# Performance work log

Measured on AMD Instinct MI355X. Metric: run time of the kernel, lower is better.

## Reference

```python
import jax, jax.numpy as jnp
import numpy as np

N = 50000      # nodes
E = 800000     # edges (avg degree 16)
NODE = 64      # node_attr_size
EDGE = 16      # edge_attr_size
H = 2          # gat_heads
C = 64         # hidden_size (per-head out channels)
F = H * C      # feature_size = 128
L = 2          # num_gat_layers
K = 10         # num_clusters
EPS = 1e-5
NEG_SLOPE = 0.2


def setup_inputs() -> dict:
    key = jax.random.key(0)
    ks = jax.random.split(key, 16)
    s = 0.05
    inp = {
        "x": jax.random.normal(ks[0], (N, NODE), jnp.float32),
        "edge_index": jax.random.randint(ks[1], (2, E), 0, N, jnp.int64 if jax.config.read('jax_enable_x64') else jnp.int32),
        "edge_attr": jax.random.normal(ks[2], (E, EDGE), jnp.float32),
        # node_feat_proj
        "Wp": jax.random.normal(ks[3], (NODE, F), jnp.float32) * s,
        "bp": jnp.zeros((F,), jnp.float32),
        # per-layer LayerNorm affine params, stacked over layers
        "ln_g": jnp.ones((L, F), jnp.float32),
        "ln_b": jnp.zeros((L, F), jnp.float32),
        # per-layer GATv2Conv params (PyG: lin_l, lin_r with bias, lin_edge no bias, att, out bias)
        "Wl": jax.random.normal(ks[4], (L, F, F), jnp.float32) * s,
        "bl": jnp.zeros((L, F), jnp.float32),
        "Wr": jax.random.normal(ks[5], (L, F, F), jnp.float32) * s,
        "br": jnp.zeros((L, F), jnp.float32),
        "We": jax.random.normal(ks[6], (L, EDGE, F), jnp.float32) * s,
        "att": jax.random.normal(ks[7], (L, H, C), jnp.float32) * s,
        "bout": jnp.zeros((L, F), jnp.float32),
        # classifier
        "Wc": jax.random.normal(ks[8], (F, K), jnp.float32) * s,
        "bc": jnp.zeros((K,), jnp.float32),
    }
    return inp


def _layer_norm(x, g, b):
    mu = jnp.mean(x, axis=-1, keepdims=True)
    var = jnp.var(x, axis=-1, keepdims=True)
    return (x - mu) * jax.lax.rsqrt(var + EPS) * g + b


def _gatv2_conv(x, src, dst, Wl, bl, Wr, br, We, att, bout):
    # x: [N, F] -> out: [N, H*C]
    xl = (x @ Wl + bl).reshape(N, H, C)          # source transform
    xr = (x @ Wr + br).reshape(N, H, C)          # target transform
    ee = (jnp.zeros(0),)  # placeholder, edge emb computed by caller closure
    return xl, xr


def reference(x, edge_index, edge_attr, Wp, bp, ln_g, ln_b, Wl, bl, Wr, br, We, att, bout, Wc, bc):
    src, dst = edge_index[0], edge_index[1]
    h = x @ Wp + bp                                   # [N, F]
    for i in range(L):
        identity = h
        hn = _layer_norm(h, ln_g[i], ln_b[i])
        xl = (hn @ Wl[i] + bl[i]).reshape(N, H, C)    # lin_l(x)  (source side)
        xr = (hn @ Wr[i] + br[i]).reshape(N, H, C)    # lin_r(x)  (target side)
        ee = (edge_attr @ We[i]).reshape(E, H, C)     # lin_edge(edge_attr)
        m = xl[src] + xr[dst] + ee                    # [E, H, C]
        m = jnp.where(m > 0, m, NEG_SLOPE * m)        # LeakyReLU(0.2)
        logits = jnp.einsum('ehc,hc->eh', m, att[i])  # [E, H]
        # segment softmax over incoming edges of each target node
        mx = jax.ops.segment_max(logits, dst, num_segments=N)
        ex = jnp.exp(logits - mx[dst])
        den = jax.ops.segment_sum(ex, dst, num_segments=N)
        alpha = ex / den[dst]                         # [E, H]
        msg = xl[src] * alpha[:, :, None]             # [E, H, C]
        agg = jax.ops.segment_sum(msg, dst, num_segments=N)  # [N, H, C]
        hg = agg.reshape(N, F) + bout[i]
        h = jax.nn.relu(hg) + identity                # relu -> dropout(eval no-op) -> residual add
    node_embeddings = h
    classification_output = h @ Wc + bc               # [N, K]
    return (classification_output, node_embeddings)
```

## Files before the change

### kernel.cpp

```cpp
#include <hip/hip_runtime.h>
#include <math.h>

#define N_NODES 50000
#define N_EDGES 800000
#define FDIM 128
#define KCLS 10

typedef float v2f __attribute__((ext_vector_type(2)));

__device__ __forceinline__ v2f pksplat(float a) { v2f r; r.x = a; r.y = a; return r; }
__device__ __forceinline__ v2f pkfma(v2f a, v2f b, v2f c) { return __builtin_elementwise_fma(a, b, c); }
__device__ __forceinline__ v2f pklrelu(v2f v) {
    v2f z = pksplat(0.f);
    v2f mx = __builtin_elementwise_max(v, z);
    v2f mn = __builtin_elementwise_min(v, z);
    return pkfma(pksplat(0.2f), mn, mx);
}
__device__ __forceinline__ int rfl(int v) { return __builtin_amdgcn_readfirstlane(v); }

__device__ __forceinline__ float half_sum32(float x) {
    int v;
    v = __builtin_amdgcn_update_dpp(0, __float_as_int(x), 0xB1, 0xF, 0xF, true);
    x += __int_as_float(v);
    v = __builtin_amdgcn_update_dpp(0, __float_as_int(x), 0x4E, 0xF, 0xF, true);
    x += __int_as_float(v);
    v = __builtin_amdgcn_update_dpp(0, __float_as_int(x), 0x124, 0xF, 0xF, true);
    x += __int_as_float(v);
    v = __builtin_amdgcn_update_dpp(0, __float_as_int(x), 0x128, 0xF, 0xF, true);
    x += __int_as_float(v);
    v = __builtin_amdgcn_ds_swizzle(__float_as_int(x), 0x401F);
    x += __int_as_float(v);
    return x;
}


__global__ void k_count(const int* __restrict__ dst, int* __restrict__ indeg, int e_total) {
    int e = blockIdx.x * 256 + threadIdx.x;
    if (e < e_total) atomicAdd(&indeg[dst[e]], 1);
}

__global__ __launch_bounds__(1024) void k_scan_block(const int* __restrict__ in, int* __restrict__ excl,
                                                     int* __restrict__ bsum, int n) {
    __shared__ int sh[1024];
    int t = threadIdx.x;
    int g = blockIdx.x * 1024 + t;
    int v = (g < n) ? in[g] : 0;
    sh[t] = v;
    __syncthreads();
    for (int d = 1; d < 1024; d <<= 1) {
        int x = (t >= d) ? sh[t - d] : 0;
        __syncthreads();
        sh[t] += x;
        __syncthreads();
    }
    if (g < n) excl[g] = sh[t] - v;
    if (t == 1023) bsum[blockIdx.x] = sh[t];
}

__global__ void k_scan_small(int* bsum, int nb) {
    if (threadIdx.x == 0 && blockIdx.x == 0) {
        int run = 0;
        for (int i = 0; i < nb; i++) { int v = bsum[i]; bsum[i] = run; run += v; }
    }
}

__global__ __launch_bounds__(1024) void k_scan_add(int* __restrict__ offs, const int* __restrict__ bsum,
                                                   int* __restrict__ cursor, int n, int e_total) {
    int g = blockIdx.x * 1024 + threadIdx.x;
    if (g < n) {
        int v = offs[g] + bsum[blockIdx.x];
        offs[g] = v;
        cursor[g] = v;
    }
    if (g == 0) offs[n] = e_total;
}

__global__ void k_scatter_fused(const int* __restrict__ src, const int* __restrict__ dst,
                                const float* __restrict__ edge_attr,
                                int* __restrict__ cursor, int* __restrict__ ssrc,
                                float* __restrict__ sea, int e_total) {
    int e = blockIdx.x * 256 + threadIdx.x;
    if (e < e_total) {
        int d = dst[e];
        int p = atomicAdd(&cursor[d], 1);
        ssrc[p] = src[e];
        const float4* ea = (const float4*)&edge_attr[(size_t)e * 16];
        float4* out = (float4*)&sea[(size_t)p * 16];
        float4 a = ea[0], b = ea[1], c = ea[2], q = ea[3];
        out[0] = a; out[1] = b; out[2] = c; out[3] = q;
    }
}

__global__ void k_scatter(const int* __restrict__ src, const int* __restrict__ dst,
                          int* __restrict__ cursor, int* __restrict__ seid, int* __restrict__ ssrc, int e_total) {
    int e = blockIdx.x * 256 + threadIdx.x;
    if (e < e_total) {
        int d = dst[e];
        int p = atomicAdd(&cursor[d], 1);
        seid[p] = e;
        ssrc[p] = src[e];
    }
}


__global__ __launch_bounds__(256) void k_ln_gemm_first(const float* __restrict__ x, const float* __restrict__ Wp,
                                                       const float* __restrict__ bp,
                                                       const float* __restrict__ lng, const float* __restrict__ lnb,
                                                       const float* __restrict__ Wl, const float* __restrict__ bl,
                                                       const float* __restrict__ Wr, const float* __restrict__ br,
                                                       float* __restrict__ h, float* __restrict__ xl,
                                                       float* __restrict__ xr, int n) {
    __shared__ float u[10240];
    __shared__ float shn[4096];
    __shared__ float smu[32], srs[32];
    int t = threadIdx.x;
    int row0 = blockIdx.x * 32;
    int nrows = min(32, n - row0);
    float* shx = u;
    float* shwp = u + 2048;

    for (int i = t; i < 2048; i += 256)
        ((float4*)shwp)[i] = ((const float4*)Wp)[i];
    for (int i = t; i < 512; i += 256) {
        int r = i >> 4;
        float4 v = make_float4(0.f, 0.f, 0.f, 0.f);
        if (r < nrows) v = ((const float4*)x)[row0 * 16 + i];
        ((float4*)shx)[i] = v;
    }
    __syncthreads();

    int tr = (t >> 5) * 4;
    int tc = (t & 31) * 4;
    {
        float acc[4][4];
        float4 b4 = *(const float4*)&bp[tc];
#pragma unroll
        for (int j = 0; j < 4; j++) { acc[j][0] = b4.x; acc[j][1] = b4.y; acc[j][2] = b4.z; acc[j][3] = b4.w; }
        for (int k = 0; k < 64; k++) {
            float4 w = *(float4*)&shwp[k * 128 + tc];
#pragma unroll
            for (int j = 0; j < 4; j++) {
                float a = shx[(tr + j) * 64 + k];
                acc[j][0] = fmaf(a, w.x, acc[j][0]);
                acc[j][1] = fmaf(a, w.y, acc[j][1]);
                acc[j][2] = fmaf(a, w.z, acc[j][2]);
                acc[j][3] = fmaf(a, w.w, acc[j][3]);
            }
        }
#pragma unroll
        for (int j = 0; j < 4; j++) {
            int r = row0 + tr + j;
            float4 o = make_float4(acc[j][0], acc[j][1], acc[j][2], acc[j][3]);
            *(float4*)&shn[(tr + j) * 128 + tc] = o;
            if (r < n) *(float4*)&h[r * 128 + tc] = o;
        }
    }
    __syncthreads();

    {
        int r = t >> 3, sl = t & 7;
        float s = 0.f, ss = 0.f;
        for (int c = sl; c < 128; c += 8) {
            float v = shn[r * 128 + c];
            s += v; ss += v * v;
        }
#pragma unroll
        for (int o = 1; o < 8; o <<= 1) { s += __shfl_xor(s, o, 64); ss += __shfl_xor(ss, o, 64); }
        if (sl == 0) {
            float mu = s * (1.f / 128.f);
            float var = ss * (1.f / 128.f) - mu * mu;
            smu[r] = mu;
            srs[r] = rsqrtf(var + 1e-5f);
        }
    }
    __syncthreads();
    for (int i = t; i < 4096; i += 256) {
        int r = i >> 7, c = i & 127;
        shn[i] = (shn[i] - smu[r]) * srs[r] * lng[c] + lnb[c];
    }

    float accl[4][4], accr[4][4];
    {
        float4 bl4 = *(const float4*)&bl[tc];
        float4 br4 = *(const float4*)&br[tc];
#pragma unroll
        for (int j = 0; j < 4; j++) {
            accl[j][0] = bl4.x; accl[j][1] = bl4.y; accl[j][2] = bl4.z; accl[j][3] = bl4.w;
            accr[j][0] = br4.x; accr[j][1] = br4.y; accr[j][2] = br4.z; accr[j][3] = br4.w;
        }
    }
    float* shwl = u;
    float* shwr = u + 4096;

    for (int kb = 0; kb < 4; kb++) {
        __syncthreads();
        for (int i = t; i < 1024; i += 256) {
            ((float4*)shwl)[i] = ((const float4*)Wl)[kb * 1024 + i];
            ((float4*)shwr)[i] = ((const float4*)Wr)[kb * 1024 + i];
        }
        __syncthreads();
#pragma unroll 8
        for (int kk = 0; kk < 32; kk++) {
            int k = kb * 32 + kk;
            float4 wl4 = *(float4*)&shwl[kk * 128 + tc];
            float4 wr4 = *(float4*)&shwr[kk * 128 + tc];
#pragma unroll
            for (int j = 0; j < 4; j++) {
                float a = shn[(tr + j) * 128 + k];
                accl[j][0] = fmaf(a, wl4.x, accl[j][0]);
                accl[j][1] = fmaf(a, wl4.y, accl[j][1]);
                accl[j][2] = fmaf(a, wl4.z, accl[j][2]);
                accl[j][3] = fmaf(a, wl4.w, accl[j][3]);
                accr[j][0] = fmaf(a, wr4.x, accr[j][0]);
                accr[j][1] = fmaf(a, wr4.y, accr[j][1]);
                accr[j][2] = fmaf(a, wr4.z, accr[j][2]);
                accr[j][3] = fmaf(a, wr4.w, accr[j][3]);
            }
        }
    }
#pragma unroll
    for (int j = 0; j < 4; j++) {
        int r = row0 + tr + j;
        if (r < n) {
            float4 ol = make_float4(accl[j][0], accl[j][1], accl[j][2], accl[j][3]);
            float4 orr = make_float4(accr[j][0], accr[j][1], accr[j][2], accr[j][3]);
            *(float4*)&xl[r * 128 + tc] = ol;
            *(float4*)&xr[r * 128 + tc] = orr;
        }
    }
}


__global__ __launch_bounds__(256) void k_ln_gemm(const float* __restrict__ h,
                                                 const float* __restrict__ lng, const float* __restrict__ lnb,
                                                 const float* __restrict__ Wl, const float* __restrict__ bl,
                                                 const float* __restrict__ Wr, const float* __restrict__ br,
                                                 float* __restrict__ xl, float* __restrict__ xr, int n) {
    __shared__ float shn[32 * 128];
    __shared__ float shwl[32 * 128];
    __shared__ float shwr[32 * 128];
    __shared__ float smu[32], srs[32];
    int t = threadIdx.x;
    int row0 = blockIdx.x * 32;
    int nrows = min(32, n - row0);

    for (int i = t; i < 1024; i += 256) {
        int r = i >> 5;
        float4 v = make_float4(0.f, 0.f, 0.f, 0.f);
        if (r < nrows) v = ((const float4*)h)[row0 * 32 + i];
        ((float4*)shn)[i] = v;
    }
    __syncthreads();

    {
        int r = t >> 3, sl = t & 7;
        float s = 0.f, ss = 0.f;
        for (int c = sl; c < 128; c += 8) {
            float v = shn[r * 128 + c];
            s += v; ss += v * v;
        }
#pragma unroll
        for (int o = 1; o < 8; o <<= 1) { s += __shfl_xor(s, o, 64); ss += __shfl_xor(ss, o, 64); }
        if (sl == 0) {
            float mu = s * (1.f / 128.f);
            float var = ss * (1.f / 128.f) - mu * mu;
            smu[r] = mu;
            srs[r] = rsqrtf(var + 1e-5f);
        }
    }
    __syncthreads();
    for (int i = t; i < 4096; i += 256) {
        int r = i >> 7, c = i & 127;
        shn[i] = (shn[i] - smu[r]) * srs[r] * lng[c] + lnb[c];
    }

    int tr = (t >> 5) * 4;
    int tc = (t & 31) * 4;
    float accl[4][4], accr[4][4];
    {
        float4 bl4 = *(const float4*)&bl[tc];
        float4 br4 = *(const float4*)&br[tc];
#pragma unroll
        for (int j = 0; j < 4; j++) {
            accl[j][0] = bl4.x; accl[j][1] = bl4.y; accl[j][2] = bl4.z; accl[j][3] = bl4.w;
            accr[j][0] = br4.x; accr[j][1] = br4.y; accr[j][2] = br4.z; accr[j][3] = br4.w;
        }
    }

    for (int kb = 0; kb < 4; kb++) {
        __syncthreads();
        for (int i = t; i < 1024; i += 256) {
            ((float4*)shwl)[i] = ((const float4*)Wl)[kb * 1024 + i];
            ((float4*)shwr)[i] = ((const float4*)Wr)[kb * 1024 + i];
        }
        __syncthreads();
#pragma unroll 8
        for (int kk = 0; kk < 32; kk++) {
            int k = kb * 32 + kk;
            float4 wl4 = *(float4*)&shwl[kk * 128 + tc];
            float4 wr4 = *(float4*)&shwr[kk * 128 + tc];
#pragma unroll
            for (int j = 0; j < 4; j++) {
                float a = shn[(tr + j) * 128 + k];
                accl[j][0] = fmaf(a, wl4.x, accl[j][0]);
                accl[j][1] = fmaf(a, wl4.y, accl[j][1]);
                accl[j][2] = fmaf(a, wl4.z, accl[j][2]);
                accl[j][3] = fmaf(a, wl4.w, accl[j][3]);
                accr[j][0] = fmaf(a, wr4.x, accr[j][0]);
                accr[j][1] = fmaf(a, wr4.y, accr[j][1]);
                accr[j][2] = fmaf(a, wr4.z, accr[j][2]);
                accr[j][3] = fmaf(a, wr4.w, accr[j][3]);
            }
        }
    }
#pragma unroll
    for (int j = 0; j < 4; j++) {
        int r = row0 + tr + j;
        if (r < n) {
            float4 ol = make_float4(accl[j][0], accl[j][1], accl[j][2], accl[j][3]);
            float4 orr = make_float4(accr[j][0], accr[j][1], accr[j][2], accr[j][3]);
            *(float4*)&xl[r * 128 + tc] = ol;
            *(float4*)&xr[r * 128 + tc] = orr;
        }
    }
}


#define AGG_BLOCKS 1280

template <bool SORTED, int G>
__device__ __forceinline__ void grpN(const float* __restrict__ xl_lane, const float* __restrict__ eattr,
                                     const int* __restrict__ seid, const int* __restrict__ ssrc,
                                     int j, v2f xr2, const v2f* we, v2f av,
                                     float& den, v2f& A) {
    v2f lx[G];
    const float* ep[G];
#pragma unroll
    for (int g = 0; g < G; g++) {
        int sn = rfl(ssrc[j + g]);
        lx[g] = *(const v2f*)(xl_lane + sn * 128);
        int r = SORTED ? (j + g) : rfl(seid[j + g]);
        ep[g] = &eattr[(size_t)r * 16];
    }
    v2f v[G];
#pragma unroll
    for (int g = 0; g < G; g++) v[g] = lx[g] + xr2;
#pragma unroll
    for (int k = 0; k < 16; k++) {
#pragma unroll
        for (int g = 0; g < G; g++) v[g] = pkfma(pksplat(ep[g][k]), we[k], v[g]);
    }
    float p[G];
#pragma unroll
    for (int g = 0; g < G; g++) {
        v2f t = pklrelu(v[g]) * av;
        p[g] = t.x + t.y;
    }
#pragma unroll
    for (int g = 0; g < G; g++) p[g] = half_sum32(p[g]);
#pragma unroll
    for (int g = 0; g < G; g++) {
        float wv = __expf(p[g]);
        den += wv;
        A = pkfma(pksplat(wv), lx[g], A);
    }
}

template <bool SORTED>
__global__ __launch_bounds__(256, 5) void k_gat_agg(const float* __restrict__ xl, const float* __restrict__ xr,
                                                    const float* __restrict__ eattr,
                                                    const int* __restrict__ offs,
                                                    const int* __restrict__ seid, const int* __restrict__ ssrc,
                                                    const float* __restrict__ We, const float* __restrict__ att,
                                                    const float* __restrict__ bout,
                                                    const float* __restrict__ hin, float* __restrict__ hout, int n) {
    int wid = threadIdx.x >> 6;
    int lane = threadIdx.x & 63;
    int gwave = blockIdx.x * 4 + wid;
    const int nwaves = AGG_BLOCKS * 4;

    int chb = (lane >> 5) * 64 + (lane & 31) * 2;
    const float* xl_lane = xl + chb;

    v2f we[16];
#pragma unroll
    for (int k = 0; k < 16; k++) we[k] = *(const v2f*)&We[k * 128 + chb];
    v2f av = *(const v2f*)&att[chb];
    v2f bo = *(const v2f*)&bout[chb];

    for (int node = gwave; node < n; node += nwaves) {
        v2f xr2 = *(const v2f*)&xr[node * 128 + chb];
        int s = rfl(offs[node]);
        int e = rfl(offs[node + 1]);
        float den = 0.f;
        v2f A = pksplat(0.f);

        int j = s;
        for (; j + 8 <= e; j += 8)
            grpN<SORTED, 8>(xl_lane, eattr, seid, ssrc, j, xr2, we, av, den, A);
        if (j + 4 <= e) {
            grpN<SORTED, 4>(xl_lane, eattr, seid, ssrc, j, xr2, we, av, den, A);
            j += 4;
        }
        for (; j < e; j++)
            grpN<SORTED, 1>(xl_lane, eattr, seid, ssrc, j, xr2, we, av, den, A);

        float inv = (e > s) ? (1.f / den) : 0.f;
        v2f hg = pkfma(A, pksplat(inv), bo);
        hg = __builtin_elementwise_max(hg, pksplat(0.f));
        v2f hv = *(const v2f*)&hin[node * 128 + chb];
        *(v2f*)&hout[node * 128 + chb] = hv + hg;
    }
}


__global__ __launch_bounds__(256) void k_cls_lite(const float* __restrict__ emb, const float* __restrict__ Wc,
                                                  const float* __restrict__ bc, float* __restrict__ out_cls, int n) {
    int wid = threadIdx.x >> 6;
    int lane = threadIdx.x & 63;
    int node = blockIdx.x * 4 + wid;
    if (node >= n) return;
    float h0 = emb[(size_t)node * 128 + lane];
    float h1 = emb[(size_t)node * 128 + 64 + lane];
    float p[10];
#pragma unroll
    for (int k = 0; k < 10; k++) p[k] = h0 * Wc[lane * 10 + k] + h1 * Wc[(64 + lane) * 10 + k];
#pragma unroll
    for (int o = 32; o; o >>= 1) {
#pragma unroll
        for (int k = 0; k < 10; k++) p[k] += __shfl_xor(p[k], o, 64);
    }
    if (lane == 0) {
#pragma unroll
        for (int k = 0; k < 10; k++) out_cls[(size_t)node * 10 + k] = p[k] + bc[k];
    }
}

extern "C" void kernel_launch(void* const* d_in, const int* in_sizes, int n_in,
                              void* d_out, int out_size, void* d_ws, size_t ws_size,
                              hipStream_t stream) {
    const float* x         = (const float*)d_in[0];
    const int*   edge_idx  = (const int*)d_in[1];
    const float* edge_attr = (const float*)d_in[2];
    const float* Wp        = (const float*)d_in[3];
    const float* bp        = (const float*)d_in[4];
    const float* lng       = (const float*)d_in[5];
    const float* lnb       = (const float*)d_in[6];
    const float* Wl        = (const float*)d_in[7];
    const float* bl        = (const float*)d_in[8];
    const float* Wr        = (const float*)d_in[9];
    const float* br        = (const float*)d_in[10];
    const float* We        = (const float*)d_in[11];
    const float* att       = (const float*)d_in[12];
    const float* bout      = (const float*)d_in[13];
    const float* Wc        = (const float*)d_in[14];
    const float* bc        = (const float*)d_in[15];

    const int N = N_NODES, E = N_EDGES;

    char* w = (char*)d_ws;
    size_t used = 0;
    auto take = [&](size_t bytes) -> void* {
        void* p = (void*)(w + used);
        used += (bytes + 255) & ~(size_t)255;
        return p;
    };
    float* h      = (float*)take((size_t)N * 128 * 4);
    float* xl     = (float*)take((size_t)N * 128 * 4);
    float* xr     = (float*)take((size_t)N * 128 * 4);
    int*   indeg  = (int*)take((size_t)N * 4);
    int*   offs   = (int*)take((size_t)(N + 1) * 4);
    int*   cursor = (int*)take((size_t)N * 4);
    int*   bsum   = (int*)take(64 * 4);
    int*   seid   = (int*)take((size_t)E * 4);
    int*   ssrc   = (int*)take((size_t)E * 4);
    float* sea    = (float*)take((size_t)E * 16 * 4);
    bool sorted_ok = (used <= ws_size);

    float* out_cls = (float*)d_out;
    float* out_emb = (float*)d_out + (size_t)N * KCLS;

    const int* srcArr = edge_idx;
    const int* dstArr = edge_idx + E;

    (void)hipMemsetAsync(indeg, 0, (size_t)N * 4, stream);
    k_count<<<(E + 255) / 256, 256, 0, stream>>>(dstArr, indeg, E);
    int NB = (N + 1023) / 1024;
    k_scan_block<<<NB, 1024, 0, stream>>>(indeg, offs, bsum, N);
    k_scan_small<<<1, 64, 0, stream>>>(bsum, NB);
    k_scan_add<<<NB, 1024, 0, stream>>>(offs, bsum, cursor, N, E);
    if (sorted_ok)
        k_scatter_fused<<<(E + 255) / 256, 256, 0, stream>>>(srcArr, dstArr, edge_attr, cursor, ssrc, sea, E);
    else
        k_scatter<<<(E + 255) / 256, 256, 0, stream>>>(srcArr, dstArr, cursor, seid, ssrc, E);

    k_ln_gemm_first<<<(N + 31) / 32, 256, 0, stream>>>(
        x, Wp, bp, lng, lnb,
        Wl, bl, Wr, br, h, xl, xr, N);
    if (sorted_ok)
        k_gat_agg<true><<<AGG_BLOCKS, 256, 0, stream>>>(
            xl, xr, sea, offs, seid, ssrc, We, att, bout, h, h, N);
    else
        k_gat_agg<false><<<AGG_BLOCKS, 256, 0, stream>>>(
            xl, xr, edge_attr, offs, seid, ssrc, We, att, bout, h, h, N);

    k_ln_gemm<<<(N + 31) / 32, 256, 0, stream>>>(
        h, lng + 128, lnb + 128,
        Wl + (size_t)128 * 128, bl + 128,
        Wr + (size_t)128 * 128, br + 128,
        xl, xr, N);
    if (sorted_ok)
        k_gat_agg<true><<<AGG_BLOCKS, 256, 0, stream>>>(
            xl, xr, sea, offs, seid, ssrc,
            We + 16 * 128, att + 128, bout + 128, h, out_emb, N);
    else
        k_gat_agg<false><<<AGG_BLOCKS, 256, 0, stream>>>(
            xl, xr, edge_attr, offs, seid, ssrc,
            We + 16 * 128, att + 128, bout + 128, h, out_emb, N);

    k_cls_lite<<<(N + 3) / 4, 256, 0, stream>>>(out_emb, Wc, bc, out_cls, N);
}
```

Measured before the change: 444.6 us.

## Split fused Wl/Wr GEMM into sequential passes and compute LayerNorm in registers

The node-transform kernels now compute the lin_l and lin_r GEMMs one after the other, each using a single shared weight tile. This halves accumulator registers and cuts shared memory to 32 KB, which should allow more resident blocks. LayerNorm statistics are computed from register-held row fragments with a DPP half-wave reduction instead of a separate shared-memory pass, and the first layer streams Wp in tiles. The cost is reading the normalized activations from shared memory twice and adding extra barriers.

```diff
diff --git a/kernel.cpp b/kernel.cpp
--- a/kernel.cpp
+++ b/kernel.cpp
@@ -103,6 +103,57 @@
 }
 
 
+__device__ __forceinline__ void gemm_pass(const float* __restrict__ W, const float* __restrict__ bias,
+                                          float* __restrict__ shw, const float* __restrict__ shn,
+                                          int t, int tr, int tc, float acc[4][4]) {
+    float4 b4 = *(const float4*)&bias[tc];
+#pragma unroll
+    for (int j = 0; j < 4; j++) { acc[j][0] = b4.x; acc[j][1] = b4.y; acc[j][2] = b4.z; acc[j][3] = b4.w; }
+    for (int kb = 0; kb < 4; kb++) {
+        __syncthreads();
+        for (int i = t; i < 1024; i += 256)
+            ((float4*)shw)[i] = ((const float4*)W)[kb * 1024 + i];
+        __syncthreads();
+#pragma unroll 8
+        for (int kk = 0; kk < 32; kk++) {
+            int k = kb * 32 + kk;
+            float4 w4 = *(float4*)&shw[kk * 128 + tc];
+#pragma unroll
+            for (int j = 0; j < 4; j++) {
+                float a = shn[(tr + j) * 128 + k];
+                acc[j][0] = fmaf(a, w4.x, acc[j][0]);
+                acc[j][1] = fmaf(a, w4.y, acc[j][1]);
+                acc[j][2] = fmaf(a, w4.z, acc[j][2]);
+                acc[j][3] = fmaf(a, w4.w, acc[j][3]);
+            }
+        }
+    }
+}
+
+__device__ __forceinline__ void ln_to_shn(float a0[4][4], const float* __restrict__ lng,
+                                          const float* __restrict__ lnb, float* __restrict__ shn,
+                                          int tr, int tc) {
+    float4 g4 = *(const float4*)&lng[tc];
+    float4 b4 = *(const float4*)&lnb[tc];
+#pragma unroll
+    for (int j = 0; j < 4; j++) {
+        float s = (a0[j][0] + a0[j][1]) + (a0[j][2] + a0[j][3]);
+        float ss = a0[j][0] * a0[j][0] + a0[j][1] * a0[j][1] + a0[j][2] * a0[j][2] + a0[j][3] * a0[j][3];
+        s = half_sum32(s);
+        ss = half_sum32(ss);
+        float mu = s * (1.f / 128.f);
+        float var = ss * (1.f / 128.f) - mu * mu;
+        float rs = rsqrtf(var + 1e-5f);
+        float4 o;
+        o.x = (a0[j][0] - mu) * rs * g4.x + b4.x;
+        o.y = (a0[j][1] - mu) * rs * g4.y + b4.y;
+        o.z = (a0[j][2] - mu) * rs * g4.z + b4.z;
+        o.w = (a0[j][3] - mu) * rs * g4.w + b4.w;
+        *(float4*)&shn[(tr + j) * 128 + tc] = o;
+    }
+}
+
+
 __global__ __launch_bounds__(256) void k_ln_gemm_first(const float* __restrict__ x, const float* __restrict__ Wp,
                                                        const float* __restrict__ bp,
                                                        const float* __restrict__ lng, const float* __restrict__ lnb,
@@ -110,123 +161,68 @@
                                                        const float* __restrict__ Wr, const float* __restrict__ br,
                                                        float* __restrict__ h, float* __restrict__ xl,
                                                        float* __restrict__ xr, int n) {
-    __shared__ float u[10240];
     __shared__ float shn[4096];
-    __shared__ float smu[32], srs[32];
+    __shared__ float shw[4096];
     int t = threadIdx.x;
     int row0 = blockIdx.x * 32;
     int nrows = min(32, n - row0);
-    float* shx = u;
-    float* shwp = u + 2048;
-
-    for (int i = t; i < 2048; i += 256)
-        ((float4*)shwp)[i] = ((const float4*)Wp)[i];
+    int tr = (t >> 5) * 4;
+    int tc = (t & 31) * 4;
+    float* shx = shn;
+
     for (int i = t; i < 512; i += 256) {
         int r = i >> 4;
         float4 v = make_float4(0.f, 0.f, 0.f, 0.f);
         if (r < nrows) v = ((const float4*)x)[row0 * 16 + i];
         ((float4*)shx)[i] = v;
     }
-    __syncthreads();
-
-    int tr = (t >> 5) * 4;
-    int tc = (t & 31) * 4;
+
+    float a0[4][4];
     {
-        float acc[4][4];
         float4 b4 = *(const float4*)&bp[tc];
 #pragma unroll
-        for (int j = 0; j < 4; j++) { acc[j][0] = b4.x; acc[j][1] = b4.y; acc[j][2] = b4.z; acc[j][3] = b4.w; }
-        for (int k = 0; k < 64; k++) {
-            float4 w = *(float4*)&shwp[k * 128 + tc];
-#pragma unroll
-            for (int j = 0; j < 4; j++) {
-                float a = shx[(tr + j) * 64 + k];
-                acc[j][0] = fmaf(a, w.x, acc[j][0]);
-                acc[j][1] = fmaf(a, w.y, acc[j][1]);
-                acc[j][2] = fmaf(a, w.z, acc[j][2]);
-                acc[j][3] = fmaf(a, w.w, acc[j][3]);
+        for (int j = 0; j < 4; j++) { a0[j][0] = b4.x; a0[j][1] = b4.y; a0[j][2] = b4.z; a0[j][3] = b4.w; }
+        for (int kb = 0; kb < 2; kb++) {
+            __syncthreads();
+            for (int i = t; i < 1024; i += 256)
+                ((float4*)shw)[i] = ((const float4*)Wp)[kb * 1024 + i];
+            __syncthreads();
+#pragma unroll 8
+            for (int kk = 0; kk < 32; kk++) {
+                int k = kb * 32 + kk;
+                float4 w4 = *(float4*)&shw[kk * 128 + tc];
+#pragma unroll
+                for (int j = 0; j < 4; j++) {
+                    float a = shx[(tr + j) * 64 + k];
+                    a0[j][0] = fmaf(a, w4.x, a0[j][0]);
+                    a0[j][1] = fmaf(a, w4.y, a0[j][1]);
+                    a0[j][2] = fmaf(a, w4.z, a0[j][2]);
+                    a0[j][3] = fmaf(a, w4.w, a0[j][3]);
+                }
             }
         }
-#pragma unroll
-        for (int j = 0; j < 4; j++) {
-            int r = row0 + tr + j;
-            float4 o = make_float4(acc[j][0], acc[j][1], acc[j][2], acc[j][3]);
-            *(float4*)&shn[(tr + j) * 128 + tc] = o;
-            if (r < n) *(float4*)&h[r * 128 + tc] = o;
-        }
     }
     __syncthreads();
 
-    {
-        int r = t >> 3, sl = t & 7;
-        float s = 0.f, ss = 0.f;
-        for (int c = sl; c < 128; c += 8) {
-            float v = shn[r * 128 + c];
-            s += v; ss += v * v;
-        }
-#pragma unroll
-        for (int o = 1; o < 8; o <<= 1) { s += __shfl_xor(s, o, 64); ss += __shfl_xor(ss, o, 64); }
-        if (sl == 0) {
-            float mu = s * (1.f / 128.f);
-            float var = ss * (1.f / 128.f) - mu * mu;
-            smu[r] = mu;
-            srs[r] = rsqrtf(var + 1e-5f);
-        }
-    }
-    __syncthreads();
-    for (int i = t; i < 4096; i += 256) {
-        int r = i >> 7, c = i & 127;
-        shn[i] = (shn[i] - smu[r]) * srs[r] * lng[c] + lnb[c];
-    }
-
-    float accl[4][4], accr[4][4];
-    {
-        float4 bl4 = *(const float4*)&bl[tc];
-        float4 br4 = *(const float4*)&br[tc];
-#pragma unroll
-        for (int j = 0; j < 4; j++) {
-            accl[j][0] = bl4.x; accl[j][1] = bl4.y; accl[j][2] = bl4.z; accl[j][3] = bl4.w;
-            accr[j][0] = br4.x; accr[j][1] = br4.y; accr[j][2] = br4.z; accr[j][3] = br4.w;
-        }
-    }
-    float* shwl = u;
-    float* shwr = u + 4096;
-
-    for (int kb = 0; kb < 4; kb++) {
-        __syncthreads();
-        for (int i = t; i < 1024; i += 256) {
-            ((float4*)shwl)[i] = ((const float4*)Wl)[kb * 1024 + i];
-            ((float4*)shwr)[i] = ((const float4*)Wr)[kb * 1024 + i];
-        }
-        __syncthreads();
-#pragma unroll 8
-        for (int kk = 0; kk < 32; kk++) {
-            int k = kb * 32 + kk;
-            float4 wl4 = *(float4*)&shwl[kk * 128 + tc];
-            float4 wr4 = *(float4*)&shwr[kk * 128 + tc];
-#pragma unroll
-            for (int j = 0; j < 4; j++) {
-                float a = shn[(tr + j) * 128 + k];
-                accl[j][0] = fmaf(a, wl4.x, accl[j][0]);
-                accl[j][1] = fmaf(a, wl4.y, accl[j][1]);
-                accl[j][2] = fmaf(a, wl4.z, accl[j][2]);
-                accl[j][3] = fmaf(a, wl4.w, accl[j][3]);
-                accr[j][0] = fmaf(a, wr4.x, accr[j][0]);
-                accr[j][1] = fmaf(a, wr4.y, accr[j][1]);
-                accr[j][2] = fmaf(a, wr4.z, accr[j][2]);
-                accr[j][3] = fmaf(a, wr4.w, accr[j][3]);
-            }
-        }
-    }
-#pragma unroll
-    for (int j = 0; j < 4; j++) {
-        int r = row0 + tr + j;
-        if (r < n) {
-            float4 ol = make_float4(accl[j][0], accl[j][1], accl[j][2], accl[j][3]);
-            float4 orr = make_float4(accr[j][0], accr[j][1], accr[j][2], accr[j][3]);
-            *(float4*)&xl[r * 128 + tc] = ol;
-            *(float4*)&xr[r * 128 + tc] = orr;
-        }
+#pragma unroll
+    for (int j = 0; j < 4; j++) {
+        int r = row0 + tr + j;
+        if (r < n) *(float4*)&h[r * 128 + tc] = make_float4(a0[j][0], a0[j][1], a0[j][2], a0[j][3]);
+    }
+    ln_to_shn(a0, lng, lnb, shn, tr, tc);
+
+    float acc[4][4];
+    gemm_pass(Wl, bl, shw, shn, t, tr, tc, acc);
+#pragma unroll
+    for (int j = 0; j < 4; j++) {
+        int r = row0 + tr + j;
+        if (r < n) *(float4*)&xl[r * 128 + tc] = make_float4(acc[j][0], acc[j][1], acc[j][2], acc[j][3]);
+    }
+    gemm_pass(Wr, br, shw, shn, t, tr, tc, acc);
+#pragma unroll
+    for (int j = 0; j < 4; j++) {
+        int r = row0 + tr + j;
+        if (r < n) *(float4*)&xr[r * 128 + tc] = make_float4(acc[j][0], acc[j][1], acc[j][2], acc[j][3]);
     }
 }
 
@@ -236,92 +232,35 @@
                                                  const float* __restrict__ Wl, const float* __restrict__ bl,
                                                  const float* __restrict__ Wr, const float* __restrict__ br,
                                                  float* __restrict__ xl, float* __restrict__ xr, int n) {
-    __shared__ float shn[32 * 128];
-    __shared__ float shwl[32 * 128];
-    __shared__ float shwr[32 * 128];
-    __shared__ float smu[32], srs[32];
+    __shared__ float shn[4096];
+    __shared__ float shw[4096];
     int t = threadIdx.x;
     int row0 = blockIdx.x * 32;
-    int nrows = min(32, n - row0);
-
-    for (int i = t; i < 1024; i += 256) {
-        int r = i >> 5;
-        float4 v = make_float4(0.f, 0.f, 0.f, 0.f);
-        if (r < nrows) v = ((const float4*)h)[row0 * 32 + i];
-        ((float4*)shn)[i] = v;
-    }
-    __syncthreads();
-
-    {
-        int r = t >> 3, sl = t & 7;
-        float s = 0.f, ss = 0.f;
-        for (int c = sl; c < 128; c += 8) {
-            float v = shn[r * 128 + c];
-            s += v; ss += v * v;
-        }
-#pragma unroll
-        for (int o = 1; o < 8; o <<= 1) { s += __shfl_xor(s, o, 64); ss += __shfl_xor(ss, o, 64); }
-        if (sl == 0) {
-            float mu = s * (1.f / 128.f);
-            float var = ss * (1.f / 128.f) - mu * mu;
-            smu[r] = mu;
-            srs[r] = rsqrtf(var + 1e-5f);
-        }
-    }
-    __syncthreads();
-    for (int i = t; i < 4096; i += 256) {
-        int r = i >> 7, c = i & 127;
-        shn[i] = (shn[i] - smu[r]) * srs[r] * lng[c] + lnb[c];
-    }
-
     int tr = (t >> 5) * 4;
     int tc = (t & 31) * 4;
-    float accl[4][4], accr[4][4];
-    {
-        float4 bl4 = *(const float4*)&bl[tc];
-        float4 br4 = *(const float4*)&br[tc];
-#pragma unroll
-        for (int j = 0; j < 4; j++) {
-            accl[j][0] = bl4.x; accl[j][1] = bl4.y; accl[j][2] = bl4.z; accl[j][3] = bl4.w;
-            accr[j][0] = br4.x; accr[j][1] = br4.y; accr[j][2] = br4.z; accr[j][3] = br4.w;
-        }
-    }
-
-    for (int kb = 0; kb < 4; kb++) {
-        __syncthreads();
-        for (int i = t; i < 1024; i += 256) {
-            ((float4*)shwl)[i] = ((const float4*)Wl)[kb * 1024 + i];
-            ((float4*)shwr)[i] = ((const float4*)Wr)[kb * 1024 + i];
-        }
-        __syncthreads();
-#pragma unroll 8
-        for (int kk = 0; kk < 32; kk++) {
-            int k = kb * 32 + kk;
-            float4 wl4 = *(float4*)&shwl[kk * 128 + tc];
-            float4 wr4 = *(float4*)&shwr[kk * 128 + tc];
-#pragma unroll
-            for (int j = 0; j < 4; j++) {
-                float a = shn[(tr + j) * 128 + k];
-                accl[j][0] = fmaf(a, wl4.x, accl[j][0]);
-                accl[j][1] = fmaf(a, wl4.y, accl[j][1]);
-                accl[j][2] = fmaf(a, wl4.z, accl[j][2]);
-                accl[j][3] = fmaf(a, wl4.w, accl[j][3]);
-                accr[j][0] = fmaf(a, wr4.x, accr[j][0]);
-                accr[j][1] = fmaf(a, wr4.y, accr[j][1]);
-                accr[j][2] = fmaf(a, wr4.z, accr[j][2]);
-                accr[j][3] = fmaf(a, wr4.w, accr[j][3]);
-            }
-        }
-    }
-#pragma unroll
-    for (int j = 0; j < 4; j++) {
-        int r = row0 + tr + j;
-        if (r < n) {
-            float4 ol = make_float4(accl[j][0], accl[j][1], accl[j][2], accl[j][3]);
-            float4 orr = make_float4(accr[j][0], accr[j][1], accr[j][2], accr[j][3]);
-            *(float4*)&xl[r * 128 + tc] = ol;
-            *(float4*)&xr[r * 128 + tc] = orr;
-        }
+
+    float a0[4][4];
+#pragma unroll
+    for (int j = 0; j < 4; j++) {
+        int r = row0 + tr + j;
+        float4 v = make_float4(0.f, 0.f, 0.f, 0.f);
+        if (r < n) v = *(const float4*)&h[(size_t)r * 128 + tc];
+        a0[j][0] = v.x; a0[j][1] = v.y; a0[j][2] = v.z; a0[j][3] = v.w;
+    }
+    ln_to_shn(a0, lng, lnb, shn, tr, tc);
+
+    float acc[4][4];
+    gemm_pass(Wl, bl, shw, shn, t, tr, tc, acc);
+#pragma unroll
+    for (int j = 0; j < 4; j++) {
+        int r = row0 + tr + j;
+        if (r < n) *(float4*)&xl[r * 128 + tc] = make_float4(acc[j][0], acc[j][1], acc[j][2], acc[j][3]);
+    }
+    gemm_pass(Wr, br, shw, shn, t, tr, tc, acc);
+#pragma unroll
+    for (int j = 0; j < 4; j++) {
+        int r = row0 + tr + j;
+        if (r < n) *(float4*)&xr[r * 128 + tc] = make_float4(acc[j][0], acc[j][1], acc[j][2], acc[j][3]);
     }
 }
 
```

Result: no change. 442.0 us (-0.6%).
